# Optimization experiments

Measured on AMD Instinct MI355X. Metric: run time of the kernel, lower is better.

Reference implementation:

```python
import jax, jax.numpy as jnp
import numpy as np
import math

B, S, D, H, R = 4, 2048, 512, 8, 8  # R = k+1 relative slots per direction


def setup_inputs() -> dict:
    key = jax.random.key(0)
    ks = jax.random.split(key, 16)
    dk = D // H
    sc = 1.0 / math.sqrt(D)
    return {
        "query": jax.random.normal(ks[0], (B, S, D), jnp.float32),
        "key": jax.random.normal(ks[1], (B, S, D), jnp.float32),
        "value": jax.random.normal(ks[2], (B, S, D), jnp.float32),
        "start_nodes": jax.random.randint(ks[3], (B, H, R, S), 0, S, jnp.int64 if jax.config.jax_enable_x64 else jnp.int32),
        "end_nodes": jax.random.randint(ks[4], (B, H, R, S), 0, S, jnp.int64 if jax.config.jax_enable_x64 else jnp.int32),
        "rel_q": jax.random.normal(ks[5], (1, H, 2 * R, dk), jnp.float32),
        "rel_k": jax.random.normal(ks[6], (1, H, 2 * R, dk), jnp.float32),
        "rel_v": jax.random.normal(ks[7], (1, H, 2 * R, dk), jnp.float32),
        "Wq": jax.random.normal(ks[8], (D, D), jnp.float32) * sc,
        "bq": jnp.zeros((D,), jnp.float32),
        "Wk": jax.random.normal(ks[9], (D, D), jnp.float32) * sc,
        "bk": jnp.zeros((D,), jnp.float32),
        "Wv": jax.random.normal(ks[10], (D, D), jnp.float32) * sc,
        "bv": jnp.zeros((D,), jnp.float32),
        "Wo": jax.random.normal(ks[11], (D, D), jnp.float32) * sc,
        "bo": jnp.zeros((D,), jnp.float32),
    }


def reference(query, key, value, start_nodes, end_nodes, rel_q, rel_k, rel_v,
              Wq, bq, Wk, bk, Wv, bv, Wo, bo):
    Bs, Ss, Ds = query.shape
    Hs = start_nodes.shape[1]
    dk = Ds // Hs

    def proj(x, W, b):
        return (x @ W.T + b).reshape(Bs, Ss, Hs, dk).transpose(0, 2, 1, 3)  # [B,H,S,dk]

    q = proj(query, Wq, bq)
    k = proj(key, Wk, bk)
    v = proj(value, Wv, bv)

    start_mask = start_nodes == -1
    sn = jnp.where(start_mask, 0, start_nodes)  # -1 padding -> 0 (masked out below)
    qidx = jnp.concatenate([end_nodes, sn], axis=2)  # [B,H,2R,S]
    kidx = jnp.concatenate([sn, end_nodes], axis=2)

    bi = jnp.arange(Bs)[:, None, None, None]
    hi = jnp.arange(Hs)[None, :, None, None]
    q_ctx = q[bi, hi, qidx]  # [B,H,2R,S,dk]
    k_ctx = k[bi, hi, kidx]
    v_ctx = v[bi, hi, kidx]

    # c2c + c2p + p2c, scale_factor = 3 (rel_q and rel_k both provided)
    scores = ((q_ctx * k_ctx).sum(-1)
              + (q_ctx * rel_k[:, :, :, None, :]).sum(-1)
              + (rel_q[:, :, :, None, :] * k_ctx).sum(-1))
    scores = scores / (3.0 * jnp.sqrt(jnp.asarray(dk, scores.dtype)))

    # mask: padded edges masked in both halves; first S flat entries always masked
    mask = jnp.concatenate([start_mask, start_mask], axis=2).reshape(Bs, Hs, -1)
    mask = mask.at[:, :, :Ss].set(True)
    sflat = jnp.exp(jnp.where(mask, -1e9, scores.reshape(Bs, Hs, -1)))  # [B,H,2R*S]

    qf = qidx.reshape(Bs, Hs, -1)
    b2 = jnp.arange(Bs)[:, None, None]
    h2 = jnp.arange(Hs)[None, :, None]
    # scatter-add softmax denominator over destination nodes, then gather back
    denom = jnp.zeros((Bs, Hs, Ss), sflat.dtype).at[b2, h2, qf].add(sflat)
    denom = jnp.where(denom == 0, -1e9, denom)
    probs = (sflat / denom[b2, h2, qf]).reshape(Bs, Hs, -1, Ss, 1)  # [B,H,2R,S,1]

    attn_v = probs * (v_ctx + rel_v[:, :, :, None, :])  # [B,H,2R,S,dk]
    out = jnp.zeros((Bs, Hs, Ss, dk), attn_v.dtype).at[b2, h2, qf].add(
        attn_v.reshape(Bs, Hs, -1, dk))  # scatter-add aggregation over edges

    out = out.transpose(0, 2, 1, 3).reshape(Bs, Ss, Ds)
    return out @ Wo.T + bo
```

## Files before the change

### kernel.cpp

```cpp
#include <hip/hip_runtime.h>
#include <math.h>

#define B_ 4
#define S_ 2048
#define D_ 512
#define H_ 8
#define R_ 8
#define DK_ 64
#define NEDGE (B_*H_*2*R_*S_)
#define EPB   (2*R_*S_)
#define ELLCAP 64
#define SCALE_ (1.0f/24.0f)

typedef __attribute__((ext_vector_type(8))) short bf16x8;
typedef __attribute__((ext_vector_type(8))) unsigned short ushort8_t;
typedef __attribute__((ext_vector_type(4))) float f32x4;

#define AS1q const __attribute__((address_space(1)))
#define AS3q __attribute__((address_space(3)))

__device__ inline unsigned short f2bf(float f) {
    unsigned u = __builtin_bit_cast(unsigned, f);
    u += 0x7fffu + ((u >> 16) & 1u);
    return (unsigned short)(u >> 16);
}
__device__ inline float bf2f(unsigned short u) {
    return __builtin_bit_cast(float, ((unsigned)u) << 16);
}

__global__ __launch_bounds__(256) void prep(
    const float* __restrict__ query, const float* __restrict__ key,
    const float* __restrict__ value,
    const float* __restrict__ Wq, const float* __restrict__ Wk,
    const float* __restrict__ Wv, const float* __restrict__ Wo,
    unsigned short* __restrict__ qc, unsigned short* __restrict__ kc,
    unsigned short* __restrict__ vc,
    unsigned short* __restrict__ wqb, unsigned short* __restrict__ wkb,
    unsigned short* __restrict__ wvb, unsigned short* __restrict__ wob)
{
    int bid = blockIdx.x;
    const float* x;
    unsigned short* y;
    size_t i;
    if (bid < 12288) {
        int z = bid >> 12;
        x = (z == 0) ? query : (z == 1) ? key : value;
        y = (z == 0) ? qc : (z == 1) ? kc : vc;
        i = ((size_t)(bid & 4095) * 256 + threadIdx.x) * 4;
    } else {
        int r = bid - 12288;
        int z = r >> 8;
        x = (z == 0) ? Wq : (z == 1) ? Wk : (z == 2) ? Wv : Wo;
        y = (z == 0) ? wqb : (z == 1) ? wkb : (z == 2) ? wvb : wob;
        i = ((size_t)(r & 255) * 256 + threadIdx.x) * 4;
    }
    float4 v = *(const float4*)&x[i];
    *(ushort4*)&y[i] = make_ushort4(f2bf(v.x), f2bf(v.y), f2bf(v.z), f2bf(v.w));
}

template<int TN>
__global__ __launch_bounds__(256) void gemm_bf16(
    const unsigned short* __restrict__ A0, const unsigned short* __restrict__ A1,
    const unsigned short* __restrict__ A2,
    const unsigned short* __restrict__ W0, const unsigned short* __restrict__ W1,
    const unsigned short* __restrict__ W2,
    const float* __restrict__ bi0, const float* __restrict__ bi1, const float* __restrict__ bi2,
    unsigned short* __restrict__ C0, unsigned short* __restrict__ C1,
    unsigned short* __restrict__ C2,
    float* __restrict__ Cf, int a_bhsd)
{
    constexpr int NFR = TN / 32;
    __shared__ unsigned short As[128 * 64];
    __shared__ unsigned short Bs[TN * 64];
    const int z = blockIdx.z;
    const unsigned short* A = (z == 0) ? A0 : (z == 1) ? A1 : A2;
    const unsigned short* W = (z == 0) ? W0 : (z == 1) ? W1 : W2;
    const float* bias        = (z == 0) ? bi0 : (z == 1) ? bi1 : bi2;
    unsigned short* C        = (z == 0) ? C0 : (z == 1) ? C1 : C2;

    const int t    = threadIdx.x;
    const int lane = t & 63;
    const int w    = t >> 6;
    const int wm   = w >> 1, wn = w & 1;
    const int m0   = blockIdx.x * 128;
    const int n0   = blockIdx.y * TN;

    const int lr    = lane >> 3;
    const int cglob = (lane & 7) ^ lr;

    f32x4 acc[4][NFR] = {};

    for (int kk = 0; kk < D_; kk += 64) {
        #pragma unroll
        for (int i = 0; i < 4; ++i) {
            int rowl = w * 32 + i * 8;
            int m = m0 + rowl + lr;
            const unsigned short* ga;
            if (a_bhsd) {
                int b = m >> 11, s = m & (S_ - 1), h = kk >> 6;
                ga = A + ((((size_t)b * H_ + h) * S_ + s) << 6) + cglob * 8;
            } else {
                ga = A + (size_t)m * D_ + kk + cglob * 8;
            }
            __builtin_amdgcn_global_load_lds((AS1q unsigned*)ga,
                (AS3q unsigned*)(As + rowl * 64), 16, 0, 0);
        }
        #pragma unroll
        for (int i = 0; i < TN / 32; ++i) {
            int rowl = w * (TN / 4) + i * 8;
            const unsigned short* gb =
                W + (size_t)(n0 + rowl + lr) * D_ + kk + cglob * 8;
            __builtin_amdgcn_global_load_lds((AS1q unsigned*)gb,
                (AS3q unsigned*)(Bs + rowl * 64), 16, 0, 0);
        }
        __syncthreads();

        #pragma unroll
        for (int ks = 0; ks < 64; ks += 32) {
            const int c0 = ks >> 3;
            bf16x8 af[4], bfr[NFR];
            #pragma unroll
            for (int mi = 0; mi < 4; ++mi) {
                int row = wm * 64 + mi * 16 + (lane & 15);
                int cp  = (c0 + (lane >> 4)) ^ (lane & 7);
                af[mi] = *(const bf16x8*)&As[row * 64 + cp * 8];
            }
            #pragma unroll
            for (int nj = 0; nj < NFR; ++nj) {
                int row = wn * (TN / 2) + nj * 16 + (lane & 15);
                int cp  = (c0 + (lane >> 4)) ^ (lane & 7);
                bfr[nj] = *(const bf16x8*)&Bs[row * 64 + cp * 8];
            }
            #pragma unroll
            for (int mi = 0; mi < 4; ++mi)
                #pragma unroll
                for (int nj = 0; nj < NFR; ++nj)
                    acc[mi][nj] = __builtin_amdgcn_mfma_f32_16x16x32_bf16(af[mi], bfr[nj], acc[mi][nj], 0, 0, 0);
        }
        __syncthreads();
    }

    #pragma unroll
    for (int mi = 0; mi < 4; ++mi) {
        #pragma unroll
        for (int nj = 0; nj < NFR; ++nj) {
            #pragma unroll
            for (int r = 0; r < 4; ++r) {
                int m = m0 + wm * 64 + mi * 16 + (lane >> 4) * 4 + r;
                int n = n0 + wn * (TN / 2) + nj * 16 + (lane & 15);
                float val = acc[mi][nj][r] + bias[n];
                if (Cf) {
                    Cf[(size_t)m * D_ + n] = val;
                } else {
                    int b = m >> 11, s = m & (S_ - 1);
                    int h = n >> 6,  d = n & 63;
                    C[((((size_t)b * H_ + h) * S_ + s) << 6) + d] = f2bf(val);
                }
            }
        }
    }
}

__global__ __launch_bounds__(256) void rel_dots(
    const unsigned short* __restrict__ q, const unsigned short* __restrict__ k_,
    const float* __restrict__ rel_q, const float* __restrict__ rel_k,
    float* __restrict__ qrk, float* __restrict__ rqk)
{
    const int t    = threadIdx.x;
    const int lane = t & 63;
    const int w    = t >> 6;
    const int n0   = blockIdx.x * 128 + w * 32;
    const int h    = (n0 >> 11) & 7;
    const int r2   = lane & 15;
    const int ch   = lane >> 4;

    bf16x8 bk2[2], bq2[2];
    #pragma unroll
    for (int ks = 0; ks < 2; ++ks) {
        const float* pk = rel_k + (((h << 4) + r2) << 6) + ks * 32 + ch * 8;
        const float* pq = rel_q + (((h << 4) + r2) << 6) + ks * 32 + ch * 8;
        f32x4 k0 = *(const f32x4*)pk, k1 = *(const f32x4*)(pk + 4);
        f32x4 q0 = *(const f32x4*)pq, q1 = *(const f32x4*)(pq + 4);
        bf16x8 bk, bq;
        #pragma unroll
        for (int i = 0; i < 4; ++i) {
            bk[i]     = (short)f2bf(k0[i]);
            bk[4 + i] = (short)f2bf(k1[i]);
            bq[i]     = (short)f2bf(q0[i]);
            bq[4 + i] = (short)f2bf(q1[i]);
        }
        bk2[ks] = bk; bq2[ks] = bq;
    }

    f32x4 aq[2] = {{0.f,0.f,0.f,0.f},{0.f,0.f,0.f,0.f}};
    f32x4 ak[2] = {{0.f,0.f,0.f,0.f},{0.f,0.f,0.f,0.f}};
    #pragma unroll
    for (int mi = 0; mi < 2; ++mi) {
        int m = n0 + mi * 16 + r2;
        #pragma unroll
        for (int ks = 0; ks < 2; ++ks) {
            bf16x8 aqf = *(const bf16x8*)&q [((size_t)m << 6) + ks * 32 + ch * 8];
            bf16x8 akf = *(const bf16x8*)&k_[((size_t)m << 6) + ks * 32 + ch * 8];
            aq[mi] = __builtin_amdgcn_mfma_f32_16x16x32_bf16(aqf, bk2[ks], aq[mi], 0, 0, 0);
            ak[mi] = __builtin_amdgcn_mfma_f32_16x16x32_bf16(akf, bq2[ks], ak[mi], 0, 0, 0);
        }
    }
    #pragma unroll
    for (int mi = 0; mi < 2; ++mi) {
        #pragma unroll
        for (int r = 0; r < 4; ++r) {
            int m = n0 + mi * 16 + (ch << 2) + r;
            qrk[((size_t)m << 4) + r2] = aq[mi][r] * SCALE_;
            rqk[((size_t)m << 4) + r2] = ak[mi][r] * SCALE_;
        }
    }
}

__global__ __launch_bounds__(1024) void attn_fused(
    const unsigned short* __restrict__ q, const unsigned short* __restrict__ k_,
    const unsigned short* __restrict__ v_,
    const float* __restrict__ qrk, const float* __restrict__ rqk,
    const float* __restrict__ rel_v,
    const int* __restrict__ start_nodes, const int* __restrict__ end_nodes,
    unsigned short* __restrict__ attn)
{
    __shared__ unsigned short ell[128 * ELLCAP];
    __shared__ int cnt[128];
    const int bi  = blockIdx.x;
    const int xcd = bi & 7;
    const int loc = bi >> 3;
    const int bh  = xcd * 4 + (loc >> 4);
    const int dlo = (loc & 15) << 7;
    const int t   = threadIdx.x;

    if (t < 128) cnt[t] = 0;
    __syncthreads();

    const int base_idx = bh * (R_ * S_);
    for (int f = S_ + t * 2; f < EPB; f += 2048) {
        int r2 = f >> 11;
        int s  = f & (S_ - 1);
        int idx = base_idx + ((r2 & 7) << 11) + s;
        int2 sn2 = *(const int2*)&start_nodes[idx];
        int2 en2 = *(const int2*)&end_nodes[idx];
        #pragma unroll
        for (int u = 0; u < 2; ++u) {
            int sn = u ? sn2.y : sn2.x;
            if (sn == -1) continue;
            int en = u ? en2.y : en2.x;
            int dst = (r2 < R_) ? en : sn;
            unsigned rel = (unsigned)(dst - dlo);
            if (rel < 128u) {
                int ki = (r2 < R_) ? sn : en;
                int pos = atomicAdd(&cnt[rel], 1);
                if (pos < ELLCAP)
                    ell[(rel << 6) + pos] = (unsigned short)((r2 << 11) | ki);
            }
        }
    }
    __syncthreads();

    const int w    = t >> 6;
    const int lane = t & 63;
    const int grp  = lane >> 3;
    const int sub  = lane & 7;
    const int h    = bh & 7;
    const size_t node_base = ((size_t)bh << 11);
    const float* qrk_bh = qrk + (node_base << 4);
    const float* rqk_bh = rqk + (node_base << 4);
    const float* rvh    = rel_v + ((size_t)(h << 4) << 6);

    for (int dd = 0; dd < 8; ++dd) {
        int dl  = dd * 16 + w;
        int dst = dlo + dl;

        ushort8_t q8 = *(const ushort8_t*)&q[((node_base + dst) << 6) + sub * 8];
        float qv[8];
        #pragma unroll
        for (int i = 0; i < 8; ++i) qv[i] = bf2f(q8[i]);
        float qrk_l = qrk_bh[((size_t)dst << 4) + (lane & 15)];

        int n = cnt[dl];
        if (n > ELLCAP) n = ELLCAP;
        int d_all = (int)ell[(dl << 6) + lane];

        float den = 0.f;
        float o[8] = {};
        #pragma unroll 2
        for (int j = 0; j < n; j += 8) {
            int slot = j + grp;
            int d = __shfl(d_all, slot);
            bool valid = slot < n;
            int ki = d & (S_ - 1);
            int r2 = (d >> 11) & 15;
            ushort8_t k8 = *(const ushort8_t*)&k_[((node_base + ki) << 6) + sub * 8];
            float p = 0.f;
            #pragma unroll
            for (int i = 0; i < 8; ++i)
                p = fmaf(bf2f(k8[i]), qv[i], p);
            p += __shfl_xor(p, 1);
            p += __shfl_xor(p, 2);
            p += __shfl_xor(p, 4);
            float tb = __shfl(qrk_l, r2) + rqk_bh[((size_t)ki << 4) + r2];
            float sf = valid ? __expf(fmaf(p, SCALE_, tb)) : 0.f;
            ushort8_t v8 = *(const ushort8_t*)&v_[((node_base + ki) << 6) + sub * 8];
            const float* rvp = rvh + (r2 << 6) + sub * 8;
            f32x4 rv0 = *(const f32x4*)rvp;
            f32x4 rv1 = *(const f32x4*)(rvp + 4);
            den += sf;
            #pragma unroll
            for (int i = 0; i < 4; ++i)
                o[i] = fmaf(sf, bf2f(v8[i]) + rv0[i], o[i]);
            #pragma unroll
            for (int i = 0; i < 4; ++i)
                o[4 + i] = fmaf(sf, bf2f(v8[4 + i]) + rv1[i], o[4 + i]);
        }
        den += __shfl_xor(den, 8); den += __shfl_xor(den, 16); den += __shfl_xor(den, 32);
        #pragma unroll
        for (int i = 0; i < 8; ++i) {
            o[i] += __shfl_xor(o[i], 8);
            o[i] += __shfl_xor(o[i], 16);
            o[i] += __shfl_xor(o[i], 32);
        }
        if (grp == 0) {
            float inv = (den > 0.f) ? 1.0f / den : 0.f;
            ushort8_t r;
            #pragma unroll
            for (int i = 0; i < 8; ++i) r[i] = f2bf(o[i] * inv);
            *(ushort8_t*)&attn[((node_base + dst) << 6) + sub * 8] = r;
        }
    }
}

extern "C" void kernel_launch(void* const* d_in, const int* in_sizes, int n_in,
                              void* d_out, int out_size, void* d_ws, size_t ws_size,
                              hipStream_t stream) {
    const float* query = (const float*)d_in[0];
    const float* key   = (const float*)d_in[1];
    const float* value = (const float*)d_in[2];
    const int* start_nodes = (const int*)d_in[3];
    const int* end_nodes   = (const int*)d_in[4];
    const float* rel_q = (const float*)d_in[5];
    const float* rel_k = (const float*)d_in[6];
    const float* rel_v = (const float*)d_in[7];
    const float* Wq = (const float*)d_in[8];
    const float* bq = (const float*)d_in[9];
    const float* Wk = (const float*)d_in[10];
    const float* bk = (const float*)d_in[11];
    const float* Wv = (const float*)d_in[12];
    const float* bv = (const float*)d_in[13];
    const float* Wo = (const float*)d_in[14];
    const float* bo = (const float*)d_in[15];
    float* out = (float*)d_out;

    const size_t NQ = (size_t)B_ * H_ * S_ * DK_;
    const size_t NW = (size_t)D_ * D_;
    unsigned short* p = (unsigned short*)d_ws;
    unsigned short* qc = p;            p += NQ;
    unsigned short* kc = p;            p += NQ;
    unsigned short* vc = p;            p += NQ;
    unsigned short* q  = p;            p += NQ;
    unsigned short* k  = p;            p += NQ;
    unsigned short* v  = p;            p += NQ;
    unsigned short* attn = p;          p += NQ;
    unsigned short* wqb = p;           p += NW;
    unsigned short* wkb = p;           p += NW;
    unsigned short* wvb = p;           p += NW;
    unsigned short* wob = p;           p += NW;
    float* qrk = (float*)qc;
    float* rqk = qrk + ((size_t)1 << 20);

    prep<<<13312, 256, 0, stream>>>(query, key, value, Wq, Wk, Wv, Wo,
                                    qc, kc, vc, wqb, wkb, wvb, wob);

    dim3 ggrid(B_ * S_ / 128, D_ / 128, 3);
    gemm_bf16<128><<<ggrid, 256, 0, stream>>>(qc, kc, vc, wqb, wkb, wvb, bq, bk, bv,
                                              q, k, v, nullptr, 0);

    rel_dots<<<512, 256, 0, stream>>>(q, k, rel_q, rel_k, qrk, rqk);

    attn_fused<<<512, 1024, 0, stream>>>(q, k, v, qrk, rqk, rel_v,
                                         start_nodes, end_nodes, attn);

    dim3 ogrid(B_ * S_ / 128, D_ / 64, 1);
    gemm_bf16<64><<<ogrid, 256, 0, stream>>>(attn, attn, attn, wob, wob, wob, bo, bo, bo,
                                             nullptr, nullptr, nullptr, out, 1);
}
```

Before: 215.8 us.

## Map one destination node per 8-lane group with prefetched edge loop

The aggregation phase now assigns each 8-lane group its own destination node instead of having a whole wavefront walk eight edges of one node across eight outer iterations. Each group loops serially over its node's edges and software-prefetches the next edge's K/V rows and bias, which removes the cross-group shuffle reductions and the outer node loop. The ELL rows are padded to a stride of 72 to reduce LDS bank conflicts, since eight groups now read different rows at once. In exchange, all groups in a wave iterate to the wave's maximum edge count, which adds divergence. The K/V loads are also serial per group, giving each lane less memory-level parallelism per iteration.

```diff
diff --git a/kernel.cpp b/kernel.cpp
--- a/kernel.cpp
+++ b/kernel.cpp
@@ -10,6 +10,7 @@
 #define NEDGE (B_*H_*2*R_*S_)
 #define EPB   (2*R_*S_)
 #define ELLCAP 64
+#define ELLSTRIDE 72
 #define SCALE_ (1.0f/24.0f)
 
 typedef __attribute__((ext_vector_type(8))) short bf16x8;
@@ -224,7 +225,7 @@
     const int* __restrict__ start_nodes, const int* __restrict__ end_nodes,
     unsigned short* __restrict__ attn)
 {
-    __shared__ unsigned short ell[128 * ELLCAP];
+    __shared__ unsigned short ell[128 * ELLSTRIDE];
     __shared__ int cnt[128];
     const int bi  = blockIdx.x;
     const int xcd = bi & 7;
@@ -254,7 +255,7 @@
                 int ki = (r2 < R_) ? sn : en;
                 int pos = atomicAdd(&cnt[rel], 1);
                 if (pos < ELLCAP)
-                    ell[(rel << 6) + pos] = (unsigned short)((r2 << 11) | ki);
+                    ell[rel * ELLSTRIDE + pos] = (unsigned short)((r2 << 11) | ki);
             }
         }
     }
@@ -262,74 +263,78 @@
 
     const int w    = t >> 6;
     const int lane = t & 63;
-    const int grp  = lane >> 3;
+    const int g    = lane >> 3;
     const int sub  = lane & 7;
+    const int dl   = w * 8 + g;
+    const int dst  = dlo + dl;
     const int h    = bh & 7;
     const size_t node_base = ((size_t)bh << 11);
     const float* qrk_bh = qrk + (node_base << 4);
     const float* rqk_bh = rqk + (node_base << 4);
     const float* rvh    = rel_v + ((size_t)(h << 4) << 6);
 
-    for (int dd = 0; dd < 8; ++dd) {
-        int dl  = dd * 16 + w;
-        int dst = dlo + dl;
-
-        ushort8_t q8 = *(const ushort8_t*)&q[((node_base + dst) << 6) + sub * 8];
-        float qv[8];
-        #pragma unroll
-        for (int i = 0; i < 8; ++i) qv[i] = bf2f(q8[i]);
-        float qrk_l = qrk_bh[((size_t)dst << 4) + (lane & 15)];
-
-        int n = cnt[dl];
-        if (n > ELLCAP) n = ELLCAP;
-        int d_all = (int)ell[(dl << 6) + lane];
-
-        float den = 0.f;
-        float o[8] = {};
-        #pragma unroll 2
-        for (int j = 0; j < n; j += 8) {
-            int slot = j + grp;
-            int d = __shfl(d_all, slot);
-            bool valid = slot < n;
-            int ki = d & (S_ - 1);
-            int r2 = (d >> 11) & 15;
-            ushort8_t k8 = *(const ushort8_t*)&k_[((node_base + ki) << 6) + sub * 8];
-            float p = 0.f;
-            #pragma unroll
-            for (int i = 0; i < 8; ++i)
-                p = fmaf(bf2f(k8[i]), qv[i], p);
-            p += __shfl_xor(p, 1);
-            p += __shfl_xor(p, 2);
-            p += __shfl_xor(p, 4);
-            float tb = __shfl(qrk_l, r2) + rqk_bh[((size_t)ki << 4) + r2];
-            float sf = valid ? __expf(fmaf(p, SCALE_, tb)) : 0.f;
-            ushort8_t v8 = *(const ushort8_t*)&v_[((node_base + ki) << 6) + sub * 8];
-            const float* rvp = rvh + (r2 << 6) + sub * 8;
-            f32x4 rv0 = *(const f32x4*)rvp;
-            f32x4 rv1 = *(const f32x4*)(rvp + 4);
-            den += sf;
-            #pragma unroll
-            for (int i = 0; i < 4; ++i)
-                o[i] = fmaf(sf, bf2f(v8[i]) + rv0[i], o[i]);
-            #pragma unroll
-            for (int i = 0; i < 4; ++i)
-                o[4 + i] = fmaf(sf, bf2f(v8[4 + i]) + rv1[i], o[4 + i]);
-        }
-        den += __shfl_xor(den, 8); den += __shfl_xor(den, 16); den += __shfl_xor(den, 32);
-        #pragma unroll
-        for (int i = 0; i < 8; ++i) {
-            o[i] += __shfl_xor(o[i], 8);
-            o[i] += __shfl_xor(o[i], 16);
-            o[i] += __shfl_xor(o[i], 32);
-        }
-        if (grp == 0) {
-            float inv = (den > 0.f) ? 1.0f / den : 0.f;
-            ushort8_t r;
-            #pragma unroll
-            for (int i = 0; i < 8; ++i) r[i] = f2bf(o[i] * inv);
-            *(ushort8_t*)&attn[((node_base + dst) << 6) + sub * 8] = r;
-        }
-    }
+    ushort8_t q8 = *(const ushort8_t*)&q[((node_base + dst) << 6) + sub * 8];
+    float qv[8];
+    #pragma unroll
+    for (int i = 0; i < 8; ++i) qv[i] = bf2f(q8[i]);
+    const float* qrow = qrk_bh + ((size_t)dst << 4);
+
+    int n = cnt[dl];
+    if (n > ELLCAP) n = ELLCAP;
+    int nmax = n;
+    nmax = max(nmax, __shfl_xor(nmax, 8));
+    nmax = max(nmax, __shfl_xor(nmax, 16));
+    nmax = max(nmax, __shfl_xor(nmax, 32));
+
+    const unsigned short* er = &ell[dl * ELLSTRIDE];
+
+    float den = 0.f;
+    float o[8] = {};
+
+    int d0 = er[0];
+    int ki = (0 < n) ? (d0 & (S_ - 1)) : 0;
+    int r2 = (0 < n) ? ((d0 >> 11) & 15) : 0;
+    ushort8_t k8 = *(const ushort8_t*)&k_[((node_base + ki) << 6) + sub * 8];
+    ushort8_t v8 = *(const ushort8_t*)&v_[((node_base + ki) << 6) + sub * 8];
+    float tb = qrow[r2] + rqk_bh[((size_t)ki << 4) + r2];
+
+    for (int j = 0; j < nmax; ++j) {
+        bool vn = (j + 1) < n;
+        int dn = er[j + 1];
+        int kin = vn ? (dn & (S_ - 1)) : 0;
+        int r2n = vn ? ((dn >> 11) & 15) : 0;
+        ushort8_t k8n = *(const ushort8_t*)&k_[((node_base + kin) << 6) + sub * 8];
+        ushort8_t v8n = *(const ushort8_t*)&v_[((node_base + kin) << 6) + sub * 8];
+        float tbn = qrow[r2n] + rqk_bh[((size_t)kin << 4) + r2n];
+
+        bool valid = j < n;
+        float p = 0.f;
+        #pragma unroll
+        for (int i = 0; i < 8; ++i)
+            p = fmaf(bf2f(k8[i]), qv[i], p);
+        p += __shfl_xor(p, 1);
+        p += __shfl_xor(p, 2);
+        p += __shfl_xor(p, 4);
+        float sf = valid ? __expf(fmaf(p, SCALE_, tb)) : 0.f;
+        const float* rvp = rvh + (r2 << 6) + sub * 8;
+        f32x4 rv0 = *(const f32x4*)rvp;
+        f32x4 rv1 = *(const f32x4*)(rvp + 4);
+        den += sf;
+        #pragma unroll
+        for (int i = 0; i < 4; ++i)
+            o[i] = fmaf(sf, bf2f(v8[i]) + rv0[i], o[i]);
+        #pragma unroll
+        for (int i = 0; i < 4; ++i)
+            o[4 + i] = fmaf(sf, bf2f(v8[4 + i]) + rv1[i], o[4 + i]);
+
+        k8 = k8n; v8 = v8n; tb = tbn; r2 = r2n;
+    }
+
+    float inv = (den > 0.f) ? 1.0f / den : 0.f;
+    ushort8_t r;
+    #pragma unroll
+    for (int i = 0; i < 8; ++i) r[i] = f2bf(o[i] * inv);
+    *(ushort8_t*)&attn[((node_base + dst) << 6) + sub * 8] = r;
 }
 
 extern "C" void kernel_launch(void* const* d_in, const int* in_sizes, int n_in,
```

New measurement: 207.9 us. 1.04x faster.
